# Optimization experiments

Measured on AMD Instinct MI355X. Metric: run time of the kernel, lower is better.

Reference implementation:

```python
import jax, jax.numpy as jnp
import numpy as np

B, S, C = 64, 1024, 512
EPS = 1e-5

def setup_inputs() -> dict:
    key = jax.random.key(0)
    k1, k2, k3 = jax.random.split(key, 3)
    x = jax.random.normal(k1, (B, S, C), dtype=jnp.float32)
    # LayerNorm affine over normalized_shape=[S, C]
    ln_w = jnp.ones((S, C), dtype=jnp.float32)
    ln_b = jnp.zeros((S, C), dtype=jnp.float32)
    # Linear(seq_len, seq_len): torch init U(-1/sqrt(S), 1/sqrt(S))
    bound = 1.0 / np.sqrt(S)
    lin_w = jax.random.uniform(k2, (S, S), jnp.float32, -bound, bound)
    lin_b = jax.random.uniform(k3, (S,), jnp.float32, -bound, bound)
    return {"x": x, "ln_w": ln_w, "ln_b": ln_b, "lin_w": lin_w, "lin_b": lin_b}

def reference(x, ln_w, ln_b, lin_w, lin_b):
    # LayerNorm over last two dims [S, C]
    mu = jnp.mean(x, axis=(1, 2), keepdims=True)
    var = jnp.mean(jnp.square(x - mu), axis=(1, 2), keepdims=True)
    h = (x - mu) * jax.lax.rsqrt(var + EPS) * ln_w + ln_b
    # permute -> [B, C, S], linear over S, relu, permute back, residual
    # fused as einsum over the seq axis directly (no explicit transpose)
    y = jnp.einsum('bsc,ts->btc', h, lin_w) + lin_b[None, :, None]
    y = jax.nn.relu(y)
    return x + y
```

## Files before the change

### kernel.cpp

```cpp
#include <hip/hip_runtime.h>
#include <stdint.h>

#define BB 64
#define SS 1024
#define CC 512
#define EPS 1e-5f

typedef __attribute__((ext_vector_type(8))) __bf16 bf16x8;
typedef __attribute__((ext_vector_type(8))) unsigned short ushort8v;
typedef __attribute__((ext_vector_type(4))) float f32x4;

__device__ __forceinline__ unsigned short f2bf(float f) {
    unsigned int u = __builtin_bit_cast(unsigned int, f);
    u += 0x7fffu + ((u >> 16) & 1u);
    return (unsigned short)(u >> 16);
}

__global__ __launch_bounds__(256) void k_convert_w(const float* __restrict__ w,
                                                   unsigned short* __restrict__ wb) {
    int i = blockIdx.x * 256 + threadIdx.x;
    float4 v = ((const float4*)w)[i];
    ushort4 o;
    o.x = f2bf(v.x); o.y = f2bf(v.y); o.z = f2bf(v.z); o.w = f2bf(v.w);
    ((ushort4*)wb)[i] = o;
}

__global__ __launch_bounds__(256) void k_stats1(const float* __restrict__ x,
                                                float* __restrict__ psum,
                                                float* __restrict__ psq) {
    int b = blockIdx.x >> 5, g = blockIdx.x & 31;
    const float4* x4 = (const float4*)(x + (size_t)b * SS * CC + (size_t)g * 16384);
    float s = 0.f, q = 0.f;
    int t = threadIdx.x;
#pragma unroll
    for (int i = 0; i < 16; ++i) {
        float4 v = x4[t + i * 256];
        s += v.x + v.y + v.z + v.w;
        q += v.x * v.x + v.y * v.y + v.z * v.z + v.w * v.w;
    }
    for (int off = 32; off; off >>= 1) {
        s += __shfl_down(s, off, 64);
        q += __shfl_down(q, off, 64);
    }
    __shared__ float ls[4], lq[4];
    int w = t >> 6;
    if ((t & 63) == 0) { ls[w] = s; lq[w] = q; }
    __syncthreads();
    if (t == 0) {
        psum[blockIdx.x] = ls[0] + ls[1] + ls[2] + ls[3];
        psq[blockIdx.x]  = lq[0] + lq[1] + lq[2] + lq[3];
    }
}

__global__ __launch_bounds__(64) void k_stats2(const float* __restrict__ psum,
                                               const float* __restrict__ psq,
                                               float* __restrict__ mu,
                                               float* __restrict__ rsig) {
    int b = blockIdx.x, t = threadIdx.x;
    float s = (t < 32) ? psum[b * 32 + t] : 0.f;
    float q = (t < 32) ? psq[b * 32 + t] : 0.f;
    for (int off = 32; off; off >>= 1) {
        s += __shfl_down(s, off, 64);
        q += __shfl_down(q, off, 64);
    }
    if (t == 0) {
        const float inv = 1.f / (float)(SS * CC);
        float m = s * inv;
        float v = q * inv - m * m;
        mu[b] = m;
        rsig[b] = rsqrtf(v + EPS);
    }
}

__global__ __launch_bounds__(256) void k_norm_t(const float* __restrict__ x,
                                                const float* __restrict__ lnw,
                                                const float* __restrict__ lnb,
                                                const float* __restrict__ muA,
                                                const float* __restrict__ rsA,
                                                unsigned short* __restrict__ Ht) {
    int idx = blockIdx.x;
    int b = idx >> 7;
    int rem = idx & 127;
    int s0 = (rem >> 3) << 6;
    int c0 = (rem & 7) << 6;
    float mu = muA[b], rs = rsA[b];
    __shared__ uint32_t lds[64 * 33];
    int t = threadIdx.x;
    int cq = t & 15, spA = t >> 4;
#pragma unroll
    for (int h = 0; h < 2; ++h) {
        int sp = spA + h * 16;
        int sl = s0 + 2 * sp;
        int cc = c0 + 4 * cq;
        size_t xb = ((size_t)b * SS + sl) * CC + cc;
        size_t lb = (size_t)sl * CC + cc;
        float4 xv0 = *(const float4*)(x + xb);
        float4 xv1 = *(const float4*)(x + xb + CC);
        float4 wv0 = *(const float4*)(lnw + lb);
        float4 wv1 = *(const float4*)(lnw + lb + CC);
        float4 bv0 = *(const float4*)(lnb + lb);
        float4 bv1 = *(const float4*)(lnb + lb + CC);
        uint32_t u0 = (uint32_t)f2bf((xv0.x - mu) * rs * wv0.x + bv0.x) |
                      ((uint32_t)f2bf((xv1.x - mu) * rs * wv1.x + bv1.x) << 16);
        uint32_t u1 = (uint32_t)f2bf((xv0.y - mu) * rs * wv0.y + bv0.y) |
                      ((uint32_t)f2bf((xv1.y - mu) * rs * wv1.y + bv1.y) << 16);
        uint32_t u2 = (uint32_t)f2bf((xv0.z - mu) * rs * wv0.z + bv0.z) |
                      ((uint32_t)f2bf((xv1.z - mu) * rs * wv1.z + bv1.z) << 16);
        uint32_t u3 = (uint32_t)f2bf((xv0.w - mu) * rs * wv0.w + bv0.w) |
                      ((uint32_t)f2bf((xv1.w - mu) * rs * wv1.w + bv1.w) << 16);
        lds[(4 * cq + 0) * 33 + sp] = u0;
        lds[(4 * cq + 1) * 33 + sp] = u1;
        lds[(4 * cq + 2) * 33 + sp] = u2;
        lds[(4 * cq + 3) * 33 + sp] = u3;
    }
    __syncthreads();
    int spq = t & 7, clA = t >> 3;
#pragma unroll
    for (int h = 0; h < 2; ++h) {
        int cl = clA + h * 32;
        uint4 v;
        v.x = lds[cl * 33 + spq * 4 + 0];
        v.y = lds[cl * 33 + spq * 4 + 1];
        v.z = lds[cl * 33 + spq * 4 + 2];
        v.w = lds[cl * 33 + spq * 4 + 3];
        size_t o = (((size_t)b * CC + c0 + cl) * SS + (size_t)s0 + spq * 8) >> 3;
        ((uint4*)Ht)[o] = v;
    }
}

__global__ __launch_bounds__(256) void k_gemm(const unsigned short* __restrict__ A,
                                              const unsigned short* __restrict__ Bt,
                                              const float* __restrict__ x,
                                              const float* __restrict__ linb,
                                              float* __restrict__ out) {
    const int b = blockIdx.z;
    const int tm = blockIdx.y;
    const int tn = blockIdx.x;
    __shared__ __align__(16) unsigned short As[128 * 32];
    __shared__ __align__(16) unsigned short Bs[128 * 32];
    const int tid = threadIdx.x;
    const int lane = tid & 63;
    const int w = tid >> 6;
    const int wm = w >> 1, wn = w & 1;
    const int quad = lane >> 4, l15 = lane & 15;

    f32x4 acc[4][4];
#pragma unroll
    for (int mi = 0; mi < 4; ++mi)
#pragma unroll
        for (int ni = 0; ni < 4; ++ni)
            acc[mi][ni] = (f32x4){0.f, 0.f, 0.f, 0.f};

    const unsigned short* Ab = A + (size_t)(tm * 128) * 1024;
    const unsigned short* Bb = Bt + ((size_t)b * 512 + tn * 128) * 1024;
    const int srow = tid >> 2;
    const int scol = (tid & 3) * 8;

    for (int k0 = 0; k0 < 1024; k0 += 32) {
        __syncthreads();
#pragma unroll
        for (int q = 0; q < 2; ++q) {
            const unsigned short* ga = Ab + (size_t)(q * 64 + srow) * 1024 + k0 + scol;
            const unsigned short* gb = Bb + (size_t)(q * 64 + srow) * 1024 + k0 + scol;
            __builtin_amdgcn_global_load_lds(
                (const __attribute__((address_space(1))) void*)ga,
                (__attribute__((address_space(3))) void*)(As + q * 2048 + w * 512),
                16, 0, 0);
            __builtin_amdgcn_global_load_lds(
                (const __attribute__((address_space(1))) void*)gb,
                (__attribute__((address_space(3))) void*)(Bs + q * 2048 + w * 512),
                16, 0, 0);
        }
        __syncthreads();

        bf16x8 av[4], bv[4];
#pragma unroll
        for (int i = 0; i < 4; ++i) {
            ushort8v a = *(const ushort8v*)&As[(wm * 64 + i * 16 + l15) * 32 + quad * 8];
            ushort8v bfr = *(const ushort8v*)&Bs[(wn * 64 + i * 16 + l15) * 32 + quad * 8];
            av[i] = __builtin_bit_cast(bf16x8, a);
            bv[i] = __builtin_bit_cast(bf16x8, bfr);
        }
#pragma unroll
        for (int mi = 0; mi < 4; ++mi)
#pragma unroll
            for (int ni = 0; ni < 4; ++ni)
                acc[mi][ni] = __builtin_amdgcn_mfma_f32_16x16x32_bf16(
                    av[mi], bv[ni], acc[mi][ni], 0, 0, 0);
    }

#pragma unroll
    for (int mi = 0; mi < 4; ++mi) {
#pragma unroll
        for (int r = 0; r < 4; ++r) {
            int tt = tm * 128 + wm * 64 + mi * 16 + quad * 4 + r;
            float lb = linb[tt];
#pragma unroll
            for (int ni = 0; ni < 4; ++ni) {
                int cc = tn * 128 + wn * 64 + ni * 16 + l15;
                size_t o = ((size_t)b * SS + tt) * CC + cc;
                float v = acc[mi][ni][r] + lb;
                v = v > 0.f ? v : 0.f;
                out[o] = x[o] + v;
            }
        }
    }
}

extern "C" void kernel_launch(void* const* d_in, const int* in_sizes, int n_in,
                              void* d_out, int out_size, void* d_ws, size_t ws_size,
                              hipStream_t stream) {
    (void)in_sizes; (void)n_in; (void)out_size; (void)ws_size;
    const float* x    = (const float*)d_in[0];
    const float* lnw  = (const float*)d_in[1];
    const float* lnb  = (const float*)d_in[2];
    const float* linw = (const float*)d_in[3];
    const float* linb = (const float*)d_in[4];
    float* out = (float*)d_out;

    char* ws = (char*)d_ws;
    unsigned short* Wb = (unsigned short*)ws;
    unsigned short* Ht = (unsigned short*)(ws + (2u << 20));
    float* psum = (float*)(ws + (66u << 20));
    float* psq  = psum + 2048;
    float* mu   = psq + 2048;
    float* rsig = mu + 64;

    k_convert_w<<<1024, 256, 0, stream>>>(linw, Wb);
    k_stats1<<<2048, 256, 0, stream>>>(x, psum, psq);
    k_stats2<<<64, 64, 0, stream>>>(psum, psq, mu, rsig);
    k_norm_t<<<8192, 256, 0, stream>>>(x, lnw, lnb, mu, rsig, Ht);
    dim3 g(4, 8, 64);
    k_gemm<<<g, 256, 0, stream>>>(Wb, Ht, x, linb, out);
}
```

Baseline: 384.1 us.

## Fold LayerNorm stats into GEMM epilogue and fuse prep passes into one kernel

The LayerNorm is rewritten algebraically: the GEMM now runs on x*ln_w without mean/rstd, and the epilogue applies rs*acc - rs*mu*(W·ln_w) + (W·ln_b + lin_b). Those two correction matrices come from a small extra GEMM. This lets a single prep kernel compute statistics, the scaled transpose and the weight conversion together, removing one full read of x. The main GEMM also gets LDS double buffering, a swizzled block order and a vectorized epilogue staged through LDS. The cost is an extra small GEMM pass and different rounding, since bf16 is applied before normalization.

```diff
diff --git a/kernel.cpp b/kernel.cpp
--- a/kernel.cpp
+++ b/kernel.cpp
@@ -16,102 +16,69 @@
     return (unsigned short)(u >> 16);
 }
 
-__global__ __launch_bounds__(256) void k_convert_w(const float* __restrict__ w,
-                                                   unsigned short* __restrict__ wb) {
-    int i = blockIdx.x * 256 + threadIdx.x;
-    float4 v = ((const float4*)w)[i];
-    ushort4 o;
-    o.x = f2bf(v.x); o.y = f2bf(v.y); o.z = f2bf(v.z); o.w = f2bf(v.w);
-    ((ushort4*)wb)[i] = o;
-}
-
-__global__ __launch_bounds__(256) void k_stats1(const float* __restrict__ x,
-                                                float* __restrict__ psum,
-                                                float* __restrict__ psq) {
-    int b = blockIdx.x >> 5, g = blockIdx.x & 31;
-    const float4* x4 = (const float4*)(x + (size_t)b * SS * CC + (size_t)g * 16384);
-    float s = 0.f, q = 0.f;
-    int t = threadIdx.x;
-#pragma unroll
-    for (int i = 0; i < 16; ++i) {
-        float4 v = x4[t + i * 256];
-        s += v.x + v.y + v.z + v.w;
-        q += v.x * v.x + v.y * v.y + v.z * v.z + v.w * v.w;
-    }
-    for (int off = 32; off; off >>= 1) {
-        s += __shfl_down(s, off, 64);
-        q += __shfl_down(q, off, 64);
-    }
+__global__ __launch_bounds__(256) void k_prep(const float* __restrict__ x,
+                                              const float* __restrict__ lnw,
+                                              const float* __restrict__ lnb,
+                                              const float* __restrict__ linw,
+                                              unsigned short* __restrict__ Wb,
+                                              unsigned short* __restrict__ Ht,
+                                              float* __restrict__ psum,
+                                              float* __restrict__ psq) {
+    const int id = blockIdx.x;
+    const int t = threadIdx.x;
+    if (id >= 8448) {
+        int i = (id - 8448) * 256 + t;
+        float4 v = ((const float4*)linw)[i];
+        ushort4 o;
+        o.x = f2bf(v.x); o.y = f2bf(v.y); o.z = f2bf(v.z); o.w = f2bf(v.w);
+        ((ushort4*)Wb)[i] = o;
+        return;
+    }
+    __shared__ uint32_t lds[64 * 33];
     __shared__ float ls[4], lq[4];
-    int w = t >> 6;
-    if ((t & 63) == 0) { ls[w] = s; lq[w] = q; }
-    __syncthreads();
-    if (t == 0) {
-        psum[blockIdx.x] = ls[0] + ls[1] + ls[2] + ls[3];
-        psq[blockIdx.x]  = lq[0] + lq[1] + lq[2] + lq[3];
-    }
-}
-
-__global__ __launch_bounds__(64) void k_stats2(const float* __restrict__ psum,
-                                               const float* __restrict__ psq,
-                                               float* __restrict__ mu,
-                                               float* __restrict__ rsig) {
-    int b = blockIdx.x, t = threadIdx.x;
-    float s = (t < 32) ? psum[b * 32 + t] : 0.f;
-    float q = (t < 32) ? psq[b * 32 + t] : 0.f;
-    for (int off = 32; off; off >>= 1) {
-        s += __shfl_down(s, off, 64);
-        q += __shfl_down(q, off, 64);
-    }
-    if (t == 0) {
-        const float inv = 1.f / (float)(SS * CC);
-        float m = s * inv;
-        float v = q * inv - m * m;
-        mu[b] = m;
-        rsig[b] = rsqrtf(v + EPS);
-    }
-}
-
-__global__ __launch_bounds__(256) void k_norm_t(const float* __restrict__ x,
-                                                const float* __restrict__ lnw,
-                                                const float* __restrict__ lnb,
-                                                const float* __restrict__ muA,
-                                                const float* __restrict__ rsA,
-                                                unsigned short* __restrict__ Ht) {
-    int idx = blockIdx.x;
-    int b = idx >> 7;
-    int rem = idx & 127;
-    int s0 = (rem >> 3) << 6;
-    int c0 = (rem & 7) << 6;
-    float mu = muA[b], rs = rsA[b];
-    __shared__ uint32_t lds[64 * 33];
-    int t = threadIdx.x;
-    int cq = t & 15, spA = t >> 4;
+    int b, rem;
+    const float* src;
+    const float* wp;
+    if (id < 8192)      { b = id >> 7; rem = id & 127; src = x + (size_t)b * SS * CC; wp = lnw; }
+    else if (id < 8320) { b = 64; rem = id - 8192; src = lnw; wp = nullptr; }
+    else                { b = 65; rem = id - 8320; src = lnb; wp = nullptr; }
+    const int s0 = (rem >> 3) << 6;
+    const int c0 = (rem & 7) << 6;
+    const int cq = t & 15, spA = t >> 4;
+    float sA = 0.f, qA = 0.f;
 #pragma unroll
     for (int h = 0; h < 2; ++h) {
         int sp = spA + h * 16;
         int sl = s0 + 2 * sp;
         int cc = c0 + 4 * cq;
-        size_t xb = ((size_t)b * SS + sl) * CC + cc;
-        size_t lb = (size_t)sl * CC + cc;
-        float4 xv0 = *(const float4*)(x + xb);
-        float4 xv1 = *(const float4*)(x + xb + CC);
-        float4 wv0 = *(const float4*)(lnw + lb);
-        float4 wv1 = *(const float4*)(lnw + lb + CC);
-        float4 bv0 = *(const float4*)(lnb + lb);
-        float4 bv1 = *(const float4*)(lnb + lb + CC);
-        uint32_t u0 = (uint32_t)f2bf((xv0.x - mu) * rs * wv0.x + bv0.x) |
-                      ((uint32_t)f2bf((xv1.x - mu) * rs * wv1.x + bv1.x) << 16);
-        uint32_t u1 = (uint32_t)f2bf((xv0.y - mu) * rs * wv0.y + bv0.y) |
-                      ((uint32_t)f2bf((xv1.y - mu) * rs * wv1.y + bv1.y) << 16);
-        uint32_t u2 = (uint32_t)f2bf((xv0.z - mu) * rs * wv0.z + bv0.z) |
-                      ((uint32_t)f2bf((xv1.z - mu) * rs * wv1.z + bv1.z) << 16);
-        uint32_t u3 = (uint32_t)f2bf((xv0.w - mu) * rs * wv0.w + bv0.w) |
-                      ((uint32_t)f2bf((xv1.w - mu) * rs * wv1.w + bv1.w) << 16);
+        size_t xb = (size_t)sl * CC + cc;
+        float4 a0 = *(const float4*)(src + xb);
+        float4 a1 = *(const float4*)(src + xb + CC);
+        float4 g0 = a0, g1 = a1;
+        if (wp) {
+            float4 w0 = *(const float4*)(wp + xb);
+            float4 w1 = *(const float4*)(wp + xb + CC);
+            g0.x = a0.x * w0.x; g0.y = a0.y * w0.y; g0.z = a0.z * w0.z; g0.w = a0.w * w0.w;
+            g1.x = a1.x * w1.x; g1.y = a1.y * w1.y; g1.z = a1.z * w1.z; g1.w = a1.w * w1.w;
+            sA += a0.x + a0.y + a0.z + a0.w + a1.x + a1.y + a1.z + a1.w;
+            qA += a0.x*a0.x + a0.y*a0.y + a0.z*a0.z + a0.w*a0.w
+                + a1.x*a1.x + a1.y*a1.y + a1.z*a1.z + a1.w*a1.w;
+        }
+        uint32_t u0 = (uint32_t)f2bf(g0.x) | ((uint32_t)f2bf(g1.x) << 16);
+        uint32_t u1 = (uint32_t)f2bf(g0.y) | ((uint32_t)f2bf(g1.y) << 16);
+        uint32_t u2 = (uint32_t)f2bf(g0.z) | ((uint32_t)f2bf(g1.z) << 16);
+        uint32_t u3 = (uint32_t)f2bf(g0.w) | ((uint32_t)f2bf(g1.w) << 16);
         lds[(4 * cq + 0) * 33 + sp] = u0;
         lds[(4 * cq + 1) * 33 + sp] = u1;
         lds[(4 * cq + 2) * 33 + sp] = u2;
         lds[(4 * cq + 3) * 33 + sp] = u3;
+    }
+    if (wp) {
+        for (int off = 32; off; off >>= 1) {
+            sA += __shfl_down(sA, off, 64);
+            qA += __shfl_down(qA, off, 64);
+        }
+        if ((t & 63) == 0) { ls[t >> 6] = sA; lq[t >> 6] = qA; }
     }
     __syncthreads();
     int spq = t & 7, clA = t >> 3;
@@ -126,18 +93,56 @@
         size_t o = (((size_t)b * CC + c0 + cl) * SS + (size_t)s0 + spq * 8) >> 3;
         ((uint4*)Ht)[o] = v;
     }
-}
-
+    if (wp && t == 0) {
+        psum[id] = ls[0] + ls[1] + ls[2] + ls[3];
+        psq[id]  = lq[0] + lq[1] + lq[2] + lq[3];
+    }
+}
+
+__global__ __launch_bounds__(128) void k_stats2(const float* __restrict__ psum,
+                                                const float* __restrict__ psq,
+                                                float* __restrict__ mu,
+                                                float* __restrict__ rsg) {
+    int b = blockIdx.x, t = threadIdx.x;
+    float s = psum[b * 128 + t];
+    float q = psq[b * 128 + t];
+    for (int off = 32; off; off >>= 1) {
+        s += __shfl_down(s, off, 64);
+        q += __shfl_down(q, off, 64);
+    }
+    __shared__ float ls[2], lq[2];
+    if ((t & 63) == 0) { ls[t >> 6] = s; lq[t >> 6] = q; }
+    __syncthreads();
+    if (t == 0) {
+        float ss = ls[0] + ls[1], qq = lq[0] + lq[1];
+        const float inv = 1.f / (float)(SS * CC);
+        float m = ss * inv;
+        float v = qq * inv - m * m;
+        mu[b] = m;
+        rsg[b] = rsqrtf(v + EPS);
+    }
+}
+
+template<bool FINAL>
 __global__ __launch_bounds__(256) void k_gemm(const unsigned short* __restrict__ A,
-                                              const unsigned short* __restrict__ Bt,
+                                              const unsigned short* __restrict__ Htall,
                                               const float* __restrict__ x,
                                               const float* __restrict__ linb,
+                                              const float* __restrict__ wl,
+                                              const float* __restrict__ blp,
+                                              const float* __restrict__ muA,
+                                              const float* __restrict__ rsA,
                                               float* __restrict__ out) {
-    const int b = blockIdx.z;
-    const int tm = blockIdx.y;
-    const int tn = blockIdx.x;
-    __shared__ __align__(16) unsigned short As[128 * 32];
-    __shared__ __align__(16) unsigned short Bs[128 * 32];
+    int b, tm, tn;
+    if constexpr (FINAL) {
+        int wg = ((blockIdx.x & 7) << 8) | (blockIdx.x >> 3);
+        b = wg >> 5;
+        int r2 = wg & 31;
+        tm = r2 >> 2; tn = r2 & 3;
+    } else {
+        tn = blockIdx.x; tm = blockIdx.y; b = 64 + blockIdx.z;
+    }
+    __shared__ __align__(16) unsigned short SM[16384];
     const int tid = threadIdx.x;
     const int lane = tid & 63;
     const int w = tid >> 6;
@@ -152,34 +157,33 @@
             acc[mi][ni] = (f32x4){0.f, 0.f, 0.f, 0.f};
 
     const unsigned short* Ab = A + (size_t)(tm * 128) * 1024;
-    const unsigned short* Bb = Bt + ((size_t)b * 512 + tn * 128) * 1024;
+    const unsigned short* Bb = Htall + ((size_t)b * 512 + tn * 128) * 1024;
     const int srow = tid >> 2;
     const int scol = (tid & 3) * 8;
 
-    for (int k0 = 0; k0 < 1024; k0 += 32) {
-        __syncthreads();
+    auto stage = [&](int buf, int k0) {
 #pragma unroll
         for (int q = 0; q < 2; ++q) {
-            const unsigned short* ga = Ab + (size_t)(q * 64 + srow) * 1024 + k0 + scol;
-            const unsigned short* gb = Bb + (size_t)(q * 64 + srow) * 1024 + k0 + scol;
             __builtin_amdgcn_global_load_lds(
-                (const __attribute__((address_space(1))) void*)ga,
-                (__attribute__((address_space(3))) void*)(As + q * 2048 + w * 512),
+                (const __attribute__((address_space(1))) void*)(Ab + (size_t)(q * 64 + srow) * 1024 + k0 + scol),
+                (__attribute__((address_space(3))) void*)(SM + buf * 4096 + q * 2048 + w * 512),
                 16, 0, 0);
             __builtin_amdgcn_global_load_lds(
-                (const __attribute__((address_space(1))) void*)gb,
-                (__attribute__((address_space(3))) void*)(Bs + q * 2048 + w * 512),
+                (const __attribute__((address_space(1))) void*)(Bb + (size_t)(q * 64 + srow) * 1024 + k0 + scol),
+                (__attribute__((address_space(3))) void*)(SM + 8192 + buf * 4096 + q * 2048 + w * 512),
                 16, 0, 0);
         }
-        __syncthreads();
-
+    };
+    auto compute = [&](int buf) {
+        const unsigned short* as = SM + buf * 4096;
+        const unsigned short* bs = SM + 8192 + buf * 4096;
         bf16x8 av[4], bv[4];
 #pragma unroll
         for (int i = 0; i < 4; ++i) {
-            ushort8v a = *(const ushort8v*)&As[(wm * 64 + i * 16 + l15) * 32 + quad * 8];
-            ushort8v bfr = *(const ushort8v*)&Bs[(wn * 64 + i * 16 + l15) * 32 + quad * 8];
+            ushort8v a  = *(const ushort8v*)&as[(wm * 64 + i * 16 + l15) * 32 + quad * 8];
+            ushort8v b2 = *(const ushort8v*)&bs[(wn * 64 + i * 16 + l15) * 32 + quad * 8];
             av[i] = __builtin_bit_cast(bf16x8, a);
-            bv[i] = __builtin_bit_cast(bf16x8, bfr);
+            bv[i] = __builtin_bit_cast(bf16x8, b2);
         }
 #pragma unroll
         for (int mi = 0; mi < 4; ++mi)
@@ -187,21 +191,74 @@
             for (int ni = 0; ni < 4; ++ni)
                 acc[mi][ni] = __builtin_amdgcn_mfma_f32_16x16x32_bf16(
                     av[mi], bv[ni], acc[mi][ni], 0, 0, 0);
-    }
-
-#pragma unroll
-    for (int mi = 0; mi < 4; ++mi) {
-#pragma unroll
-        for (int r = 0; r < 4; ++r) {
-            int tt = tm * 128 + wm * 64 + mi * 16 + quad * 4 + r;
-            float lb = linb[tt];
-#pragma unroll
-            for (int ni = 0; ni < 4; ++ni) {
-                int cc = tn * 128 + wn * 64 + ni * 16 + l15;
-                size_t o = ((size_t)b * SS + tt) * CC + cc;
-                float v = acc[mi][ni][r] + lb;
-                v = v > 0.f ? v : 0.f;
-                out[o] = x[o] + v;
+    };
+
+    stage(0, 0);
+    __syncthreads();
+    for (int j = 0; j < 15; ++j) {
+        int k0 = j * 64;
+        stage(1, k0 + 32);
+        compute(0);
+        __syncthreads();
+        stage(0, k0 + 64);
+        compute(1);
+        __syncthreads();
+    }
+    stage(1, 992);
+    compute(0);
+    __syncthreads();
+    compute(1);
+
+    if constexpr (FINAL) {
+        __syncthreads();
+        const float rsv  = rsA[b];
+        const float rsmu = rsv * muA[b];
+        float* eps = (float*)SM + (w << 11);
+#pragma unroll
+        for (int ch = 0; ch < 2; ++ch) {
+#pragma unroll
+            for (int m2 = 0; m2 < 2; ++m2) {
+                int mi = ch * 2 + m2;
+#pragma unroll
+                for (int ni = 0; ni < 4; ++ni)
+#pragma unroll
+                    for (int r = 0; r < 4; ++r)
+                        eps[(m2 * 16 + quad * 4 + r) * 64 + ni * 16 + l15] = acc[mi][ni][r];
+            }
+#pragma unroll
+            for (int jj = 0; jj < 8; ++jj) {
+                int row = jj * 4 + quad;
+                int tt = tm * 128 + wm * 64 + ch * 32 + row;
+                int cc = tn * 128 + wn * 64 + l15 * 4;
+                size_t o2 = (size_t)tt * 512 + cc;
+                size_t o  = ((size_t)b * 1024 + tt) * 512 + cc;
+                f32x4 v   = *(f32x4*)&eps[row * 64 + l15 * 4];
+                f32x4 wv  = *(const f32x4*)&wl[o2];
+                f32x4 bv2 = *(const f32x4*)&blp[o2];
+                f32x4 xv  = *(const f32x4*)&x[o];
+                f32x4 ov;
+#pragma unroll
+                for (int e = 0; e < 4; ++e) {
+                    float vv = rsv * v[e] - rsmu * wv[e] + bv2[e];
+                    vv = vv > 0.f ? vv : 0.f;
+                    ov[e] = xv[e] + vv;
+                }
+                *(f32x4*)&out[o] = ov;
+            }
+        }
+    } else {
+        int z = b - 64;
+#pragma unroll
+        for (int mi = 0; mi < 4; ++mi) {
+#pragma unroll
+            for (int r = 0; r < 4; ++r) {
+                int tt = tm * 128 + wm * 64 + mi * 16 + quad * 4 + r;
+                float add = z ? linb[tt] : 0.f;
+#pragma unroll
+                for (int ni = 0; ni < 4; ++ni) {
+                    int cc = tn * 128 + wn * 64 + ni * 16 + l15;
+                    out[((size_t)z * 1024 + tt) * 512 + cc] = acc[mi][ni][r] + add;
+                }
             }
         }
     }
@@ -221,15 +278,16 @@
     char* ws = (char*)d_ws;
     unsigned short* Wb = (unsigned short*)ws;
     unsigned short* Ht = (unsigned short*)(ws + (2u << 20));
-    float* psum = (float*)(ws + (66u << 20));
-    float* psq  = psum + 2048;
-    float* mu   = psq + 2048;
-    float* rsig = mu + 64;
-
-    k_convert_w<<<1024, 256, 0, stream>>>(linw, Wb);
-    k_stats1<<<2048, 256, 0, stream>>>(x, psum, psq);
-    k_stats2<<<64, 64, 0, stream>>>(psum, psq, mu, rsig);
-    k_norm_t<<<8192, 256, 0, stream>>>(x, lnw, lnb, mu, rsig, Ht);
-    dim3 g(4, 8, 64);
-    k_gemm<<<g, 256, 0, stream>>>(Wb, Ht, x, linb, out);
-}
+    float* wlblp = (float*)(ws + (68u << 20));
+    float* psum  = (float*)(ws + (72u << 20));
+    float* psq   = psum + 8192;
+    float* mu    = psq + 8192;
+    float* rsg   = mu + 64;
+
+    k_prep<<<9472, 256, 0, stream>>>(x, lnw, lnb, linw, Wb, Ht, psum, psq);
+    k_stats2<<<64, 128, 0, stream>>>(psum, psq, mu, rsg);
+    k_gemm<false><<<dim3(4, 8, 2), 256, 0, stream>>>(Wb, Ht, nullptr, linb,
+                                                     nullptr, nullptr, nullptr, nullptr, wlblp);
+    k_gemm<true><<<2048, 256, 0, stream>>>(Wb, Ht, x, nullptr,
+                                           wlblp, wlblp + 512 * 1024, mu, rsg, out);
+}
```

Result: slower. 395.0 us (+2.8%).
